# Kernel optimization log

Measured on AMD Instinct MI355X. Metric: run time of the kernel, lower is better.

## Reference

```python
import jax, jax.numpy as jnp
import numpy as np

B, BAG, H, C = 512, 32, 1024, 53
EPS = 1e-8  # torch F.cosine_similarity denominator clamp


def setup_inputs() -> dict:
    key = jax.random.key(0)
    ks = jax.random.split(key, 5)
    return {
        "sent_reps": jax.random.normal(ks[0], (B, BAG, H), jnp.float32),
        "aug_sent_reps": jax.random.normal(ks[1], (B, BAG, H), jnp.float32),
        "rel_table": jax.random.normal(ks[2], (C, H), jnp.float32),
        "cls_w": jax.random.normal(ks[3], (C, H), jnp.float32) * 0.02,
        "cls_b": jnp.zeros((C,), jnp.float32),
        "labels": jax.random.randint(ks[4], (B,), 0, C),
        "temperature": jnp.asarray(0.1, jnp.float32),
    }


def _cl(rep, aug, bag_rep, T):
    # rep, aug: (B, bag, H); bag_rep: (B, H)
    nr = jnp.linalg.norm(rep, axis=-1)        # (B, bag)
    na = jnp.linalg.norm(aug, axis=-1)        # (B, bag)
    nb = jnp.linalg.norm(bag_rep, axis=-1)    # (B,)
    pos_sim = jnp.sum(rep * aug, axis=-1) / jnp.maximum(nr * na, EPS)  # (B, bag)
    pos = jnp.exp(pos_sim / T)
    # pair[c, j, b] = cos(rep[b, j], bag_rep[c])  -- matches torch permute/broadcast chain
    dots = jnp.einsum('bjh,ch->cjb', rep, bag_rep)               # (B, bag, B)
    denom = jnp.maximum(nb[:, None, None] * nr.T[None], EPS)      # (B, bag, B)
    pair = dots / denom
    idx = jnp.arange(rep.shape[0])
    axis_sim = pair[idx, :, idx]                                  # (B, bag): cos(rep[b,j], bag_rep[b])
    neg = jnp.exp(pair / T).sum(axis=2) - jnp.exp(axis_sim / T)   # (B, bag)
    return jnp.mean(-jnp.log(pos / (pos + neg)))


def reference(sent_reps, aug_sent_reps, rel_table, cls_w, cls_b, labels, temperature):
    # Selective attention per bag (scope slices are uniform bags of size BAG -> vectorized)
    rel = rel_table[labels]                                        # (B, H)
    scale = jnp.sqrt(jnp.asarray(H, sent_reps.dtype))
    scores = jnp.einsum('bh,bjh->bj', rel, sent_reps) / scale      # (B, bag)
    alphas = jax.nn.softmax(scores, axis=-1)
    bag_reps = jnp.einsum('bj,bjh->bh', alphas, sent_reps)         # (B, H)
    bag_out = bag_reps @ cls_w.T + cls_b                           # (B, C)  (dropout in eval = identity)
    cl_loss = _cl(sent_reps, aug_sent_reps, bag_reps, temperature)
    return bag_out, cl_loss
```

## Files before the change

kernel.cpp:

```cpp
#include <hip/hip_runtime.h>
#include <hip/hip_bf16.h>


typedef __bf16 bf16x8 __attribute__((ext_vector_type(8)));
typedef __bf16 bf16x4 __attribute__((ext_vector_type(4)));
typedef float  f32x4  __attribute__((ext_vector_type(4)));

__device__ inline float wsum(float v) {
    #pragma unroll
    for (int off = 32; off > 0; off >>= 1) v += __shfl_xor(v, off, 64);
    return v;
}

__device__ inline void gll16(const void* g, void* l) {
    __builtin_amdgcn_global_load_lds((const __attribute__((address_space(1))) void*)g,
                                     (__attribute__((address_space(3))) void*)l, 16, 0, 0);
}

__global__ __launch_bounds__(256) void k0_cvt(const float* __restrict__ w, __bf16* __restrict__ wb,
                                              float* __restrict__ nbsq)
{
    int i = blockIdx.x * 256 + threadIdx.x;
    wb[i] = (i < 53 * 1024) ? (__bf16)w[i] : (__bf16)0.0f;
    if (i < 512) nbsq[i] = 0.0f;
}

__global__ __launch_bounds__(256) void ka(
    const float* __restrict__ sent, const float* __restrict__ aug,
    const float* __restrict__ rel_table, const int* __restrict__ labels,
    __bf16* __restrict__ repb, float* __restrict__ nr, float* __restrict__ pos_sim,
    float* __restrict__ scoreg)
{
    const int w = threadIdx.x >> 6, lane = threadIdx.x & 63;
    const int row = blockIdx.x * 4 + w;
    const int b = row >> 5;
    const size_t rbase = (size_t)row * 1024;
    const float* srow = sent + rbase;
    const float* arow = aug + rbase;
    const float* relp = rel_table + (size_t)labels[b] * 1024;

    float P = 0.f, R = 0.f, A = 0.f, D = 0.f;
    #pragma unroll
    for (int i = 0; i < 4; i++) {
        const int h = i * 256 + lane * 4;
        f32x4 v  = *(const f32x4*)(srow + h);
        f32x4 a  = *(const f32x4*)(arow + h);
        f32x4 rl = *(const f32x4*)(relp + h);
        P += v.x * rl.x + v.y * rl.y + v.z * rl.z + v.w * rl.w;
        R += v.x * v.x + v.y * v.y + v.z * v.z + v.w * v.w;
        A += a.x * a.x + a.y * a.y + a.z * a.z + a.w * a.w;
        D += v.x * a.x + v.y * a.y + v.z * a.z + v.w * a.w;
        bf16x4 vb = { (__bf16)v.x, (__bf16)v.y, (__bf16)v.z, (__bf16)v.w };
        *(bf16x4*)(repb + rbase + h) = vb;
    }
    #pragma unroll
    for (int off = 32; off > 0; off >>= 1) {
        P += __shfl_xor(P, off, 64);
        R += __shfl_xor(R, off, 64);
        A += __shfl_xor(A, off, 64);
        D += __shfl_xor(D, off, 64);
    }
    if (lane == 0) {
        scoreg[row] = P * (1.0f / 32.0f);
        float nrv = sqrtf(R), nav = sqrtf(A);
        nr[row] = nrv;
        pos_sim[row] = D / fmaxf(nrv * nav, 1e-8f);
    }
}

__global__ __launch_bounds__(256) void kb(
    const __bf16* __restrict__ repb, const float* __restrict__ scoreg,
    __bf16* __restrict__ bagb, float* __restrict__ nbsq)
{
    __shared__ float alphaS[32];
    const int b = blockIdx.x, t = threadIdx.x;
    if (t < 32) {
        float sj = scoreg[b * 32 + t];
        float m = sj;
        #pragma unroll
        for (int off = 16; off > 0; off >>= 1) m = fmaxf(m, __shfl_xor(m, off, 32));
        float e = __expf(sj - m);
        float sum = e;
        #pragma unroll
        for (int off = 16; off > 0; off >>= 1) sum += __shfl_xor(sum, off, 32);
        alphaS[t] = e / sum;
    }
    __syncthreads();

    f32x4 acc = {};
    const __bf16* base = repb + (size_t)b * 32 * 1024 + t * 4;
    #pragma unroll 8
    for (int jj = 0; jj < 32; jj++) {
        bf16x4 v = *(const bf16x4*)(base + jj * 1024);
        const float al = alphaS[jj];
        acc.x += al * (float)v.x;
        acc.y += al * (float)v.y;
        acc.z += al * (float)v.z;
        acc.w += al * (float)v.w;
    }
    bf16x4 bb = { (__bf16)acc.x, (__bf16)acc.y, (__bf16)acc.z, (__bf16)acc.w };
    *(bf16x4*)(bagb + (size_t)b * 1024 + t * 4) = bb;

    float q = acc.x * acc.x + acc.y * acc.y + acc.z * acc.z + acc.w * acc.w;
    q = wsum(q);
    if ((t & 63) == 0) atomicAdd(&nbsq[b], q);
}

__global__ __launch_bounds__(256) void k3m(
    const __bf16* __restrict__ bagb, const __bf16* __restrict__ cwb,
    const float* __restrict__ bias, float* __restrict__ out)
{
    __shared__ __align__(16) __bf16 Al[2 * 2048];
    __shared__ __align__(16) __bf16 Bl[2 * 2048];
    const int r0 = blockIdx.x * 64;
    const int t = threadIdx.x, lane = t & 63, w = t >> 6;
    const int m = lane & 15, quad = lane >> 4;
    f32x4 acc[4] = {};

    const int i0 = t * 8;
    const int row0 = i0 >> 5, kk0 = i0 & 31;
    const __bf16* gA = bagb + (size_t)(r0 + row0) * 1024 + kk0;
    const __bf16* gB = cwb + (size_t)row0 * 1024 + kk0;

    for (int k0 = 0; k0 < 1024; k0 += 64) {
        __syncthreads();
        gll16(gA + k0,      Al + i0);
        gll16(gA + k0 + 32, Al + 2048 + i0);
        gll16(gB + k0,      Bl + i0);
        gll16(gB + k0 + 32, Bl + 2048 + i0);
        __syncthreads();
        #pragma unroll
        for (int ks = 0; ks < 2; ks++) {
            bf16x8 a = *(const bf16x8*)(&Al[ks * 2048 + (w * 16 + m) * 32 + quad * 8]);
            #pragma unroll
            for (int n = 0; n < 4; n++) {
                bf16x8 bf = *(const bf16x8*)(&Bl[ks * 2048 + (n * 16 + m) * 32 + quad * 8]);
                acc[n] = __builtin_amdgcn_mfma_f32_16x16x32_bf16(a, bf, acc[n], 0, 0, 0);
            }
        }
    }
    #pragma unroll
    for (int n = 0; n < 4; n++) {
        const int c = n * 16 + m;
        if (c < 53) {
            #pragma unroll
            for (int i = 0; i < 4; i++) {
                const int r = r0 + w * 16 + quad * 4 + i;
                out[(size_t)r * 53 + c] = acc[n][i] + bias[c];
            }
        }
    }
}

__global__ __launch_bounds__(256) void k4_gemm(
    const __bf16* __restrict__ repb, const __bf16* __restrict__ bagb,
    const float* __restrict__ nr, const float* __restrict__ nbsq,
    const float* __restrict__ temp, float* __restrict__ partial, float* __restrict__ diag)
{
    __shared__ __align__(16) __bf16 Al[128 * 32];
    __shared__ __align__(16) __bf16 Bl[128 * 32];
    __shared__ float negp[2][32][128];
    const int bid = blockIdx.x;
    const int xcd = bid & 7, slot = bid >> 3;
    const int cb = slot & 3, rb = (slot >> 2) * 8 + xcd;
    const int r0 = rb * 128, c0 = cb * 128;
    const int t = threadIdx.x, lane = t & 63, w = t >> 6;
    const int m = lane & 15, quad = lane >> 4;
    const int wr0 = (w & 1) * 64, wc0 = (w >> 1) * 64;
    const int half = w & 1;

    #pragma unroll
    for (int z = 0; z < 32; z++) ((float*)negp)[z * 256 + t] = 0.f;

    f32x4 acc[4][4] = {};

    const int i0 = t * 8, i1 = 2048 + t * 8;
    const int row0 = i0 >> 5, kk0 = i0 & 31;
    const int row1 = i1 >> 5, kk1 = i1 & 31;
    const __bf16* gA0 = repb + (size_t)(r0 + row0) * 1024 + kk0;
    const __bf16* gA1 = repb + (size_t)(r0 + row1) * 1024 + kk1;
    const __bf16* gB0 = bagb + (size_t)(c0 + row0) * 1024 + kk0;
    const __bf16* gB1 = bagb + (size_t)(c0 + row1) * 1024 + kk1;

    for (int k0 = 0; k0 < 1024; k0 += 32) {
        __syncthreads();
        gll16(gA0 + k0, Al + i0);
        gll16(gA1 + k0, Al + i1);
        gll16(gB0 + k0, Bl + i0);
        gll16(gB1 + k0, Bl + i1);
        __syncthreads();
        bf16x8 a[4], bf[4];
        #pragma unroll
        for (int i = 0; i < 4; i++) a[i]  = *(const bf16x8*)(&Al[(wr0 + i * 16 + m) * 32 + quad * 8]);
        #pragma unroll
        for (int n = 0; n < 4; n++) bf[n] = *(const bf16x8*)(&Bl[(wc0 + n * 16 + m) * 32 + quad * 8]);
        #pragma unroll
        for (int i = 0; i < 4; i++)
            #pragma unroll
            for (int n = 0; n < 4; n++)
                acc[i][n] = __builtin_amdgcn_mfma_f32_16x16x32_bf16(a[i], bf[n], acc[i][n], 0, 0, 0);
    }

    const float invT = 1.0f / *temp;
    float nrv[16];
    #pragma unroll
    for (int i = 0; i < 4; i++)
        #pragma unroll
        for (int g = 0; g < 4; g++)
            nrv[i * 4 + g] = nr[r0 + wr0 + i * 16 + quad * 4 + g];

    #pragma unroll
    for (int n = 0; n < 4; n++) {
        const int c_local = wc0 + n * 16 + m;
        const int cg = c0 + c_local;
        const float nbv = sqrtf(nbsq[cg]);
        #pragma unroll
        for (int i = 0; i < 2; i++) {
            #pragma unroll
            for (int g = 0; g < 4; g++) {
                const int jj = i * 16 + quad * 4 + g;
                const int rg0 = r0 + wr0 + i * 16 + quad * 4 + g;
                const int rg2 = rg0 + 32;
                float e0 = __expf(acc[i][n][g]     / fmaxf(nbv * nrv[i * 4 + g],       1e-8f) * invT);
                float e2 = __expf(acc[i + 2][n][g] / fmaxf(nbv * nrv[(i + 2) * 4 + g], 1e-8f) * invT);
                negp[half][jj][c_local] = e0 + e2;
                if ((rg0 >> 5) == cg) diag[(size_t)cg * 32 + jj] = e0;
                if ((rg2 >> 5) == cg) diag[(size_t)cg * 32 + jj] = e2;
            }
        }
    }
    __syncthreads();

    float* pout = partial + (size_t)rb * 32 * 512 + c0;
    #pragma unroll
    for (int v = 0; v < 4; v++) {
        const int idx = v * 1024 + t * 4;
        const int jj = idx >> 7, cl = idx & 127;
        f32x4 a = *(const f32x4*)(&negp[0][jj][cl]);
        f32x4 bq = *(const f32x4*)(&negp[1][jj][cl]);
        f32x4 s = a + bq;
        *(f32x4*)(pout + (size_t)jj * 512 + cl) = s;
    }
}

__global__ __launch_bounds__(256) void k5_neg(
    const float* __restrict__ partial, const float* __restrict__ diag,
    const float* __restrict__ pos_sim, const float* __restrict__ temp,
    float* __restrict__ bsums)
{
    const int ct = blockIdx.x & 7, j = blockIdx.x >> 3;
    const int t = threadIdx.x, lane = t & 63, w = t >> 6;
    const int bsub = t >> 4;
    const int cidx = t & 15;
    f32x4 acc = {};
    #pragma unroll 4
    for (int r = 0; r < 8; r++) {
        const int rb = bsub * 8 + r;
        f32x4 v = *(const f32x4*)(partial + ((size_t)rb * 32 + j) * 512 + ct * 64 + cidx * 4);
        acc += v;
    }
    #pragma unroll
    for (int k = 0; k < 4; k++) {
        acc[k] += __shfl_xor(acc[k], 16, 64);
        acc[k] += __shfl_xor(acc[k], 32, 64);
    }
    __shared__ float red[4][64];
    if (lane < 16) {
        #pragma unroll
        for (int k = 0; k < 4; k++) red[w][lane * 4 + k] = acc[k];
    }
    __syncthreads();

    if (t < 64) {
        const int c = ct * 64 + t;
        float S = red[0][t] + red[1][t] + red[2][t] + red[3][t];
        S -= diag[(size_t)c * 32 + j];
        const float invT = 1.0f / *temp;
        const float lp = pos_sim[(c << 5) + j] * invT;
        float term = logf(__expf(lp) + S) - lp;
        term = wsum(term);
        if (t == 0) bsums[blockIdx.x] = term;
    }
}

__global__ __launch_bounds__(256) void k6_final(const float* __restrict__ bsums, float* __restrict__ loss)
{
    const int t = threadIdx.x;
    float v = bsums[t];
    v = wsum(v);
    __shared__ float r[4];
    if ((t & 63) == 0) r[t >> 6] = v;
    __syncthreads();
    if (t == 0) *loss = (r[0] + r[1] + r[2] + r[3]) * (1.0f / 16384.0f);
}

extern "C" void kernel_launch(void* const* d_in, const int* in_sizes, int n_in,
                              void* d_out, int out_size, void* d_ws, size_t ws_size,
                              hipStream_t stream)
{
    const float* sent = (const float*)d_in[0];
    const float* aug  = (const float*)d_in[1];
    const float* rel  = (const float*)d_in[2];
    const float* clsw = (const float*)d_in[3];
    const float* clsb = (const float*)d_in[4];
    const int*   lab  = (const int*)d_in[5];
    const float* temp = (const float*)d_in[6];
    float* out = (float*)d_out;

    char* ws = (char*)d_ws;
    __bf16* bagb    = (__bf16*)(ws);
    float*  nbsq    = (float*)(ws + (1u << 20));
    float*  nr      = (float*)(ws + (1u << 20) + 64 * 1024);
    float*  pos     = (float*)(ws + (1u << 20) + 128 * 1024);
    __bf16* cwb     = (__bf16*)(ws + (1u << 20) + 192 * 1024);
    float*  scoreg  = (float*)(ws + (1u << 20) + 320 * 1024);
    float*  bsums   = (float*)(ws + (2u << 20));
    float*  diag    = (float*)(ws + (2u << 20) + 64 * 1024);
    __bf16* repb    = (__bf16*)(ws + (4u << 20));
    float*  partial = (float*)(ws + (36u << 20));

    k0_cvt  <<<256, 256, 0, stream>>>(clsw, cwb, nbsq);
    ka      <<<4096, 256, 0, stream>>>(sent, aug, rel, lab, repb, nr, pos, scoreg);
    kb      <<<512, 256, 0, stream>>>(repb, scoreg, bagb, nbsq);
    k3m     <<<8, 256, 0, stream>>>(bagb, cwb, clsb, out);
    k4_gemm <<<512, 256, 0, stream>>>(repb, bagb, nr, nbsq, temp, partial, diag);
    k5_neg  <<<256, 256, 0, stream>>>(partial, diag, pos, temp, bsums);
    k6_final<<<1, 256, 0, stream>>>(bsums, out + 27136);
}
```

Measured before the change: 214.1 us.

## Fold small kernels into neighbors, cutting launches from seven to four

```diff
diff --git a/kernel.cpp b/kernel.cpp
--- a/kernel.cpp
+++ b/kernel.cpp
@@ -15,56 +15,76 @@
 __device__ inline void gll16(const void* g, void* l) {
     __builtin_amdgcn_global_load_lds((const __attribute__((address_space(1))) void*)g,
                                      (__attribute__((address_space(3))) void*)l, 16, 0, 0);
-}
-
-__global__ __launch_bounds__(256) void k0_cvt(const float* __restrict__ w, __bf16* __restrict__ wb,
-                                              float* __restrict__ nbsq)
-{
-    int i = blockIdx.x * 256 + threadIdx.x;
-    wb[i] = (i < 53 * 1024) ? (__bf16)w[i] : (__bf16)0.0f;
-    if (i < 512) nbsq[i] = 0.0f;
 }
 
 __global__ __launch_bounds__(256) void ka(
     const float* __restrict__ sent, const float* __restrict__ aug,
     const float* __restrict__ rel_table, const int* __restrict__ labels,
     __bf16* __restrict__ repb, float* __restrict__ nr, float* __restrict__ pos_sim,
-    float* __restrict__ scoreg)
-{
-    const int w = threadIdx.x >> 6, lane = threadIdx.x & 63;
-    const int row = blockIdx.x * 4 + w;
-    const int b = row >> 5;
-    const size_t rbase = (size_t)row * 1024;
-    const float* srow = sent + rbase;
-    const float* arow = aug + rbase;
-    const float* relp = rel_table + (size_t)labels[b] * 1024;
-
-    float P = 0.f, R = 0.f, A = 0.f, D = 0.f;
+    float* __restrict__ scoreg,
+    const float* __restrict__ clsw, __bf16* __restrict__ cwb,
+    float* __restrict__ nbsq, float* __restrict__ loss)
+{
+    const int t = threadIdx.x;
+    if (blockIdx.x < 256) {
+        const int i = blockIdx.x * 256 + t;
+        cwb[i] = (i < 53 * 1024) ? (__bf16)clsw[i] : (__bf16)0.0f;
+    } else if (blockIdx.x == 256) {
+        nbsq[t] = 0.0f; nbsq[256 + t] = 0.0f;
+        if (t == 0) *loss = 0.0f;
+    }
+
+    const int w = t >> 6, lane = t & 63;
+    const int rp = blockIdx.x * 8 + w * 2;
+    const size_t rb0 = (size_t)rp * 1024, rb1 = rb0 + 1024;
+    const float* s0 = sent + rb0;
+    const float* s1 = sent + rb1;
+    const float* a0 = aug + rb0;
+    const float* a1 = aug + rb1;
+    const float* relp = rel_table + (size_t)labels[rp >> 5] * 1024;
+
+    f32x4 v0[4], v1[4], x0[4], x1[4], rl[4];
     #pragma unroll
     for (int i = 0; i < 4; i++) {
         const int h = i * 256 + lane * 4;
-        f32x4 v  = *(const f32x4*)(srow + h);
-        f32x4 a  = *(const f32x4*)(arow + h);
-        f32x4 rl = *(const f32x4*)(relp + h);
-        P += v.x * rl.x + v.y * rl.y + v.z * rl.z + v.w * rl.w;
-        R += v.x * v.x + v.y * v.y + v.z * v.z + v.w * v.w;
-        A += a.x * a.x + a.y * a.y + a.z * a.z + a.w * a.w;
-        D += v.x * a.x + v.y * a.y + v.z * a.z + v.w * a.w;
-        bf16x4 vb = { (__bf16)v.x, (__bf16)v.y, (__bf16)v.z, (__bf16)v.w };
-        *(bf16x4*)(repb + rbase + h) = vb;
+        v0[i] = *(const f32x4*)(s0 + h);
+        v1[i] = *(const f32x4*)(s1 + h);
+        x0[i] = *(const f32x4*)(a0 + h);
+        x1[i] = *(const f32x4*)(a1 + h);
+        rl[i] = *(const f32x4*)(relp + h);
+    }
+    float P0 = 0.f, R0 = 0.f, A0 = 0.f, D0 = 0.f;
+    float P1 = 0.f, R1 = 0.f, A1 = 0.f, D1 = 0.f;
+    #pragma unroll
+    for (int i = 0; i < 4; i++) {
+        const int h = i * 256 + lane * 4;
+        #pragma unroll
+        for (int e = 0; e < 4; e++) {
+            P0 += v0[i][e] * rl[i][e];  R0 += v0[i][e] * v0[i][e];
+            A0 += x0[i][e] * x0[i][e];  D0 += v0[i][e] * x0[i][e];
+            P1 += v1[i][e] * rl[i][e];  R1 += v1[i][e] * v1[i][e];
+            A1 += x1[i][e] * x1[i][e];  D1 += v1[i][e] * x1[i][e];
+        }
+        bf16x4 w0 = { (__bf16)v0[i][0], (__bf16)v0[i][1], (__bf16)v0[i][2], (__bf16)v0[i][3] };
+        bf16x4 w1 = { (__bf16)v1[i][0], (__bf16)v1[i][1], (__bf16)v1[i][2], (__bf16)v1[i][3] };
+        *(bf16x4*)(repb + rb0 + h) = w0;
+        *(bf16x4*)(repb + rb1 + h) = w1;
     }
     #pragma unroll
     for (int off = 32; off > 0; off >>= 1) {
-        P += __shfl_xor(P, off, 64);
-        R += __shfl_xor(R, off, 64);
-        A += __shfl_xor(A, off, 64);
-        D += __shfl_xor(D, off, 64);
+        P0 += __shfl_xor(P0, off, 64); R0 += __shfl_xor(R0, off, 64);
+        A0 += __shfl_xor(A0, off, 64); D0 += __shfl_xor(D0, off, 64);
+        P1 += __shfl_xor(P1, off, 64); R1 += __shfl_xor(R1, off, 64);
+        A1 += __shfl_xor(A1, off, 64); D1 += __shfl_xor(D1, off, 64);
     }
     if (lane == 0) {
-        scoreg[row] = P * (1.0f / 32.0f);
-        float nrv = sqrtf(R), nav = sqrtf(A);
-        nr[row] = nrv;
-        pos_sim[row] = D / fmaxf(nrv * nav, 1e-8f);
+        scoreg[rp]     = P0 * (1.0f / 32.0f);
+        scoreg[rp + 1] = P1 * (1.0f / 32.0f);
+        float n0 = sqrtf(R0), m0 = sqrtf(A0);
+        float n1 = sqrtf(R1), m1 = sqrtf(A1);
+        nr[rp] = n0; nr[rp + 1] = n1;
+        pos_sim[rp]     = D0 / fmaxf(n0 * m0, 1e-8f);
+        pos_sim[rp + 1] = D1 / fmaxf(n1 * m1, 1e-8f);
     }
 }
 
@@ -106,66 +126,61 @@
     if ((t & 63) == 0) atomicAdd(&nbsq[b], q);
 }
 
-__global__ __launch_bounds__(256) void k3m(
-    const __bf16* __restrict__ bagb, const __bf16* __restrict__ cwb,
-    const float* __restrict__ bias, float* __restrict__ out)
-{
-    __shared__ __align__(16) __bf16 Al[2 * 2048];
-    __shared__ __align__(16) __bf16 Bl[2 * 2048];
-    const int r0 = blockIdx.x * 64;
-    const int t = threadIdx.x, lane = t & 63, w = t >> 6;
-    const int m = lane & 15, quad = lane >> 4;
-    f32x4 acc[4] = {};
-
-    const int i0 = t * 8;
-    const int row0 = i0 >> 5, kk0 = i0 & 31;
-    const __bf16* gA = bagb + (size_t)(r0 + row0) * 1024 + kk0;
-    const __bf16* gB = cwb + (size_t)row0 * 1024 + kk0;
-
-    for (int k0 = 0; k0 < 1024; k0 += 64) {
-        __syncthreads();
-        gll16(gA + k0,      Al + i0);
-        gll16(gA + k0 + 32, Al + 2048 + i0);
-        gll16(gB + k0,      Bl + i0);
-        gll16(gB + k0 + 32, Bl + 2048 + i0);
-        __syncthreads();
-        #pragma unroll
-        for (int ks = 0; ks < 2; ks++) {
-            bf16x8 a = *(const bf16x8*)(&Al[ks * 2048 + (w * 16 + m) * 32 + quad * 8]);
-            #pragma unroll
-            for (int n = 0; n < 4; n++) {
-                bf16x8 bf = *(const bf16x8*)(&Bl[ks * 2048 + (n * 16 + m) * 32 + quad * 8]);
-                acc[n] = __builtin_amdgcn_mfma_f32_16x16x32_bf16(a, bf, acc[n], 0, 0, 0);
-            }
-        }
-    }
-    #pragma unroll
-    for (int n = 0; n < 4; n++) {
-        const int c = n * 16 + m;
-        if (c < 53) {
-            #pragma unroll
-            for (int i = 0; i < 4; i++) {
-                const int r = r0 + w * 16 + quad * 4 + i;
-                out[(size_t)r * 53 + c] = acc[n][i] + bias[c];
-            }
-        }
-    }
-}
-
 __global__ __launch_bounds__(256) void k4_gemm(
     const __bf16* __restrict__ repb, const __bf16* __restrict__ bagb,
     const float* __restrict__ nr, const float* __restrict__ nbsq,
-    const float* __restrict__ temp, float* __restrict__ partial, float* __restrict__ diag)
-{
-    __shared__ __align__(16) __bf16 Al[128 * 32];
-    __shared__ __align__(16) __bf16 Bl[128 * 32];
-    __shared__ float negp[2][32][128];
+    const float* __restrict__ temp, float* __restrict__ partial, float* __restrict__ diag,
+    const __bf16* __restrict__ cwb, const float* __restrict__ bias, float* __restrict__ out)
+{
+    __shared__ __align__(16) char smem[49152];
+    __bf16* Al = (__bf16*)smem;
+    __bf16* Bl = (__bf16*)(smem + 8192);
     const int bid = blockIdx.x;
+    const int t = threadIdx.x, lane = t & 63, w = t >> 6;
+    const int m = lane & 15, quad = lane >> 4;
+
+    if (bid >= 512) {
+        const int r0 = (bid - 512) * 64;
+        f32x4 acc[4] = {};
+        const int i0 = t * 8;
+        const int row0 = i0 >> 5, kk0 = i0 & 31;
+        const __bf16* gA = bagb + (size_t)(r0 + row0) * 1024 + kk0;
+        const __bf16* gB = cwb + (size_t)row0 * 1024 + kk0;
+        for (int k0 = 0; k0 < 1024; k0 += 64) {
+            __syncthreads();
+            gll16(gA + k0,      Al + i0);
+            gll16(gA + k0 + 32, Al + 2048 + i0);
+            gll16(gB + k0,      Bl + i0);
+            gll16(gB + k0 + 32, Bl + 2048 + i0);
+            __syncthreads();
+            #pragma unroll
+            for (int ks = 0; ks < 2; ks++) {
+                bf16x8 a = *(const bf16x8*)(&Al[ks * 2048 + (w * 16 + m) * 32 + quad * 8]);
+                #pragma unroll
+                for (int n = 0; n < 4; n++) {
+                    bf16x8 bf = *(const bf16x8*)(&Bl[ks * 2048 + (n * 16 + m) * 32 + quad * 8]);
+                    acc[n] = __builtin_amdgcn_mfma_f32_16x16x32_bf16(a, bf, acc[n], 0, 0, 0);
+                }
+            }
+        }
+        #pragma unroll
+        for (int n = 0; n < 4; n++) {
+            const int c = n * 16 + m;
+            if (c < 53) {
+                #pragma unroll
+                for (int i = 0; i < 4; i++) {
+                    const int r = r0 + w * 16 + quad * 4 + i;
+                    out[(size_t)r * 53 + c] = acc[n][i] + bias[c];
+                }
+            }
+        }
+        return;
+    }
+
+    float (*negp)[32][128] = (float (*)[32][128])(smem + 16384);
     const int xcd = bid & 7, slot = bid >> 3;
     const int cb = slot & 3, rb = (slot >> 2) * 8 + xcd;
     const int r0 = rb * 128, c0 = cb * 128;
-    const int t = threadIdx.x, lane = t & 63, w = t >> 6;
-    const int m = lane & 15, quad = lane >> 4;
     const int wr0 = (w & 1) * 64, wc0 = (w >> 1) * 64;
     const int half = w & 1;
 
@@ -246,7 +261,7 @@
 __global__ __launch_bounds__(256) void k5_neg(
     const float* __restrict__ partial, const float* __restrict__ diag,
     const float* __restrict__ pos_sim, const float* __restrict__ temp,
-    float* __restrict__ bsums)
+    float* __restrict__ loss)
 {
     const int ct = blockIdx.x & 7, j = blockIdx.x >> 3;
     const int t = threadIdx.x, lane = t & 63, w = t >> 6;
@@ -279,19 +294,8 @@
         const float lp = pos_sim[(c << 5) + j] * invT;
         float term = logf(__expf(lp) + S) - lp;
         term = wsum(term);
-        if (t == 0) bsums[blockIdx.x] = term;
-    }
-}
-
-__global__ __launch_bounds__(256) void k6_final(const float* __restrict__ bsums, float* __restrict__ loss)
-{
-    const int t = threadIdx.x;
-    float v = bsums[t];
-    v = wsum(v);
-    __shared__ float r[4];
-    if ((t & 63) == 0) r[t >> 6] = v;
-    __syncthreads();
-    if (t == 0) *loss = (r[0] + r[1] + r[2] + r[3]) * (1.0f / 16384.0f);
+        if (t == 0) atomicAdd(loss, term * (1.0f / 16384.0f));
+    }
 }
 
 extern "C" void kernel_launch(void* const* d_in, const int* in_sizes, int n_in,
@@ -314,16 +318,16 @@
     float*  pos     = (float*)(ws + (1u << 20) + 128 * 1024);
     __bf16* cwb     = (__bf16*)(ws + (1u << 20) + 192 * 1024);
     float*  scoreg  = (float*)(ws + (1u << 20) + 320 * 1024);
-    float*  bsums   = (float*)(ws + (2u << 20));
     float*  diag    = (float*)(ws + (2u << 20) + 64 * 1024);
     __bf16* repb    = (__bf16*)(ws + (4u << 20));
     float*  partial = (float*)(ws + (36u << 20));
 
-    k0_cvt  <<<256, 256, 0, stream>>>(clsw, cwb, nbsq);
-    ka      <<<4096, 256, 0, stream>>>(sent, aug, rel, lab, repb, nr, pos, scoreg);
-    kb      <<<512, 256, 0, stream>>>(repb, scoreg, bagb, nbsq);
-    k3m     <<<8, 256, 0, stream>>>(bagb, cwb, clsb, out);
-    k4_gemm <<<512, 256, 0, stream>>>(repb, bagb, nr, nbsq, temp, partial, diag);
-    k5_neg  <<<256, 256, 0, stream>>>(partial, diag, pos, temp, bsums);
-    k6_final<<<1, 256, 0, stream>>>(bsums, out + 27136);
-}
+    float* loss = out + 27136;
+
+    ka     <<<2048, 256, 0, stream>>>(sent, aug, rel, lab, repb, nr, pos, scoreg,
+                                      clsw, cwb, nbsq, loss);
+    kb     <<<512, 256, 0, stream>>>(repb, scoreg, bagb, nbsq);
+    k4_gemm<<<520, 256, 0, stream>>>(repb, bagb, nr, nbsq, temp, partial, diag,
+                                     cwb, clsb, out);
+    k5_neg <<<256, 256, 0, stream>>>(partial, diag, pos, temp, loss);
+}
```

New measurement: 213.7 us. About the same (-0.2%).
